# Optimization experiments

Hardware: AMD Instinct MI355X
Metric: run time of the kernel (lower is better)

Reference implementation:

```python
import jax, jax.numpy as jnp
import numpy as np

B, T = 128, 512
V, E, H, A, L = 50000, 256, 512, 64, 2


def setup_inputs() -> dict:
    key = jax.random.key(0)
    ks = jax.random.split(key, 16)
    token_ids = jax.random.randint(ks[0], (B, T), 0, V, dtype=jnp.int32)
    # lengths must be >= 2 so that the source's (len-1)-1 index is valid
    lengths = jnp.clip(jax.random.randint(ks[1], (B,), 0, T, dtype=jnp.int32), 4, T)
    s = 0.05
    inp = {
        "token_ids": token_ids,
        "lengths": lengths,
        "embedding": jax.random.normal(ks[2], (V, E), jnp.float32) * s,
        "Wt": jax.random.normal(ks[3], (A, E), jnp.float32) * s,   # tokens_linear
        "bt": jax.random.normal(ks[4], (A,), jnp.float32) * s,
        "Wq": jax.random.normal(ks[5], (A, H), jnp.float32) * s,   # query_linear
        "bq": jax.random.normal(ks[6], (A,), jnp.float32) * s,
        "v": jax.random.normal(ks[7], (A,), jnp.float32) * s,      # attention_linear weight
        "bv": jax.random.normal(ks[8], (), jnp.float32) * s,       # attention_linear bias
        "gru_Wih0": jax.random.normal(ks[9], (3 * H, A), jnp.float32) * s,
        "gru_Whh0": jax.random.normal(ks[10], (3 * H, H), jnp.float32) * s,
        "gru_bih0": jax.random.normal(ks[11], (3 * H,), jnp.float32) * s,
        "gru_bhh0": jax.random.normal(ks[12], (3 * H,), jnp.float32) * s,
        "gru_Wih1": jax.random.normal(ks[13], (3 * H, H), jnp.float32) * s,
        "gru_Whh1": jax.random.normal(ks[14], (3 * H, H), jnp.float32) * s,
        "gru_bih1": jax.random.normal(ks[15], (3 * H,), jnp.float32) * s,
        "gru_bhh1": jax.random.normal(jax.random.fold_in(key, 99), (3 * H,), jnp.float32) * s,
    }
    return inp


def _gru_cell(x, h, Wih, Whh, bih, bhh):
    gi = x @ Wih.T + bih      # [B, 3H]
    gh = h @ Whh.T + bhh      # [B, 3H]
    i_r, i_z, i_n = jnp.split(gi, 3, axis=-1)
    h_r, h_z, h_n = jnp.split(gh, 3, axis=-1)
    r = jax.nn.sigmoid(i_r + h_r)
    z = jax.nn.sigmoid(i_z + h_z)
    n = jnp.tanh(i_n + r * h_n)
    return (1.0 - z) * n + z * h


def reference(token_ids, lengths, embedding, Wt, bt, Wq, bq, v, bv,
              gru_Wih0, gru_Whh0, gru_bih0, gru_bhh0,
              gru_Wih1, gru_Whh1, gru_bih1, gru_bhh1):
    x = embedding[token_ids]                 # [B, T, E]
    tp = jnp.einsum('bte,ae->bta', x, Wt) + bt   # tokens_linear, [B, T, A]
    pos = jnp.arange(T)

    def step(h, i):
        # query = hidden_state[-1] (zeros at step 0, matching hidden_state=None)
        q = h[-1] @ Wq.T + bq                # [B, A]
        s = jnp.tanh(tp + q[:, None, :]) @ v + bv   # [B, T]
        s = jnp.where(pos[None, :] <= i, s, -jnp.inf)  # growing prefix
        attn = jax.nn.softmax(s, axis=1)
        ctx = jnp.einsum('bt,bta->ba', attn, tp)     # [B, A]
        h0 = _gru_cell(ctx, h[0], gru_Wih0, gru_Whh0, gru_bih0, gru_bhh0)
        h1 = _gru_cell(h0, h[1], gru_Wih1, gru_Whh1, gru_bih1, gru_bhh1)
        return jnp.stack([h0, h1]), h1

    h_init = jnp.zeros((L, B, H), tp.dtype)
    _, outs = jax.lax.scan(step, h_init, jnp.arange(T))   # outs: [T, B, H]
    # source: sequence_lengths = len-1, then index sequence_lengths-1 = len-2
    idx = jnp.clip(lengths - 2, 0, T - 1)
    result = outs[idx, jnp.arange(B)]                     # [B, H]
    return result
```

## Files before the change

kernel.cpp:

```cpp
#include <hip/hip_runtime.h>

#define NB 128
#define NT 512
#define NE 256
#define NH 512
#define NA 64
#define NG 8
#define GB 16

typedef short bf16x8 __attribute__((ext_vector_type(8)));
typedef float f32x4 __attribute__((ext_vector_type(4)));
typedef unsigned short u16x8 __attribute__((ext_vector_type(8)));
typedef unsigned long long u64;

__device__ __forceinline__ unsigned short f2bf(float f){
  unsigned u = __builtin_bit_cast(unsigned, f);
  u = u + 0x7fffu + ((u >> 16) & 1u);
  return (unsigned short)(u >> 16);
}
__device__ __forceinline__ float bf2f(unsigned short h){
  unsigned u = ((unsigned)h) << 16;
  return __builtin_bit_cast(float, u);
}
__device__ __forceinline__ bf16x8 packbf2(f32x4 a, f32x4 b){
  bf16x8 r;
  r[0]=(short)f2bf(a[0]); r[1]=(short)f2bf(a[1]); r[2]=(short)f2bf(a[2]); r[3]=(short)f2bf(a[3]);
  r[4]=(short)f2bf(b[0]); r[5]=(short)f2bf(b[1]); r[6]=(short)f2bf(b[2]); r[7]=(short)f2bf(b[3]);
  return r;
}
__device__ __forceinline__ bf16x8 loadB_f32(const float* p){
  f32x4 a = *(const f32x4*)p;
  f32x4 b = *(const f32x4*)(p + 4);
  return packbf2(a, b);
}
#define MFMA(a,b,c) __builtin_amdgcn_mfma_f32_16x16x32_bf16(a,b,c,0,0,0)

__device__ __forceinline__ float fsig(float x){
  return __builtin_amdgcn_rcpf(1.f + __expf(-x));
}
__device__ __forceinline__ float ftanh(float x){
  float e2 = __expf(2.f * x);
  return 1.f - 2.f * __builtin_amdgcn_rcpf(e2 + 1.f);
}

__device__ __forceinline__ u64 aload(const u64* p){
  return __hip_atomic_load(p, __ATOMIC_RELAXED, __HIP_MEMORY_SCOPE_AGENT);
}
__device__ __forceinline__ void fire(u64* p, u64 v){
  (void)__hip_atomic_exchange(p, v, __ATOMIC_RELAXED, __HIP_MEMORY_SCOPE_AGENT);
}
__device__ __forceinline__ u64 packh(unsigned sq, float a, float b){
  return ((u64)sq << 32) | ((u64)f2bf(b) << 16) | (u64)f2bf(a);
}
__device__ __forceinline__ u64 packf(unsigned sq, float a){
  return ((u64)sq << 32) | (u64)__builtin_bit_cast(unsigned, a);
}

__global__ __launch_bounds__(256) void k_tp(
    const int* __restrict__ tok, const float* __restrict__ emb,
    const float* __restrict__ Wt, const float* __restrict__ bt,
    unsigned short* __restrict__ tp)
{
  const int lane = threadIdx.x & 63;
  const int w = threadIdx.x >> 6;
  const int m16 = lane & 15, quad = lane >> 4;

  bf16x8 wfq[8][4];
#pragma unroll
  for (int kc = 0; kc < 8; kc++)
#pragma unroll
    for (int nt = 0; nt < 4; nt++)
      wfq[kc][nt] = loadB_f32(Wt + (nt*16 + m16)*NE + kc*32 + quad*8);

  float btv[4];
#pragma unroll
  for (int nt = 0; nt < 4; nt++) btv[nt] = bt[nt*16 + m16];

  const int gw = blockIdx.x * 4 + w;
#pragma unroll 1
  for (int it = 0; it < 4; it++){
    const int pt = gw * 4 + it;
    const int pos = pt*16 + m16;
    const long row = (long)tok[pos];
    const float* xrow = emb + row * NE;
    f32x4 acc[4] = {{0,0,0,0},{0,0,0,0},{0,0,0,0},{0,0,0,0}};
#pragma unroll
    for (int kc = 0; kc < 8; kc++){
      bf16x8 af = loadB_f32(xrow + kc*32 + quad*8);
#pragma unroll
      for (int nt = 0; nt < 4; nt++)
        acc[nt] = MFMA(af, wfq[kc][nt], acc[nt]);
    }
#pragma unroll
    for (int nt = 0; nt < 4; nt++)
#pragma unroll
      for (int r = 0; r < 4; r++){
        int posr = pt*16 + quad*4 + r;
        tp[(long)posr * NA + nt*16 + m16] = f2bf(acc[nt][r] + btv[nt]);
      }
  }
}

__global__ __launch_bounds__(256) void k_pack(
    const float* __restrict__ Wq, unsigned short* __restrict__ blob)
{
  const int lane = threadIdx.x & 63, wv = threadIdx.x >> 6;
  const int m16 = lane & 15, quad = lane >> 4;
#pragma unroll
  for (int kc = 0; kc < 16; kc++){
    bf16x8 t = loadB_f32(Wq + (long)(wv*16 + m16)*NH + kc*32 + quad*8);
    *(bf16x8*)&blob[((wv*16 + kc)*64 + lane)*8] = t;
  }
}

struct KArgs {
  const int* len;
  const float* bq; const float* v; const float* bv;
  const float* Wih0; const float* Whh0; const float* bih0; const float* bhh0;
  const float* Wih1; const float* Whh1; const float* bih1; const float* bhh1;
  const unsigned short* tp;
  const unsigned short* wqblob;
  u64* hbuf;
  u64* cbuf;
  float* out;
};

__device__ __forceinline__ void stage_poll(const u64* __restrict__ buf, unsigned sq,
                                           unsigned short (*hs)[64][8], int tid){
  const int lane = tid & 63, wv = tid >> 6;
  const int b = lane & 15, q8 = lane >> 4;
#pragma unroll
  for (int c = 0; c < 4; c++){
    const int kc = wv*4 + c;
    const u64* u0 = buf + (kc*16 + q8*4)*16 + b;
    u64 x0, x1, x2, x3;
    for (;;){
      x0 = aload(u0);      x1 = aload(u0 + 16);
      x2 = aload(u0 + 32); x3 = aload(u0 + 48);
      if ((unsigned)(x0>>32)==sq && (unsigned)(x1>>32)==sq &&
          (unsigned)(x2>>32)==sq && (unsigned)(x3>>32)==sq) break;
      __builtin_amdgcn_s_sleep(1);
    }
    u16x8 d;
    d[0]=(unsigned short)x0; d[1]=(unsigned short)(x0>>16);
    d[2]=(unsigned short)x1; d[3]=(unsigned short)(x1>>16);
    d[4]=(unsigned short)x2; d[5]=(unsigned short)(x2>>16);
    d[6]=(unsigned short)x3; d[7]=(unsigned short)(x3>>16);
    *(u16x8*)&hs[kc][lane][0] = d;
  }
}

__global__ __launch_bounds__(256, 1) void k_main(KArgs A_)
{
  const int tid = threadIdx.x, lane = tid & 63, w = tid >> 6;
  const int g = blockIdx.x & 7, m = blockIdx.x >> 3;
  const int m16 = lane & 15, quad = lane >> 4;

  __shared__ __attribute__((aligned(16))) unsigned short h0s[16][64][8];
  __shared__ __attribute__((aligned(16))) unsigned short h1s[16][64][8];
  __shared__ __attribute__((aligned(16))) float dslab[6][256];
  __shared__ __attribute__((aligned(16))) float qs[16][68];
  __shared__ __attribute__((aligned(16))) float cslab[4][64];
  __shared__ float cden[4];
  __shared__ __attribute__((aligned(16))) unsigned short ctxf[64][16];

  u64* hb = A_.hbuf + (long)g * (4*4096);
  u64* cb = A_.cbuf + (long)g * (2*2*16*72);
  const int b0 = g * GB;

  bf16x8 wf[48], wih0f[2];
  float bhh0v[4], bih0v[4], bhh1v[4], bih1v[4];
  if (w < 3){
    const int r0 = w * NH + m * 16;
#pragma unroll
    for (int kc = 0; kc < 16; kc++){
      wf[kc]    = loadB_f32(A_.Whh0 + (long)(r0 + m16)*NH + kc*32 + quad*8);
      wf[16+kc] = loadB_f32(A_.Whh1 + (long)(r0 + m16)*NH + kc*32 + quad*8);
      wf[32+kc] = loadB_f32(A_.Wih1 + (long)(r0 + m16)*NH + kc*32 + quad*8);
    }
#pragma unroll
    for (int kc = 0; kc < 2; kc++)
      wih0f[kc] = loadB_f32(A_.Wih0 + (r0 + m16)*NA + kc*32 + quad*8);
#pragma unroll
    for (int r = 0; r < 4; r++){
      int d = r0 + quad*4 + r;
      bhh0v[r] = A_.bhh0[d]; bih0v[r] = A_.bih0[d];
      bhh1v[r] = A_.bhh1[d]; bih1v[r] = A_.bih1[d];
    }
  }
  float bqw[4];
#pragma unroll
  for (int r = 0; r < 4; r++) bqw[r] = A_.bq[w*16 + quad*4 + r];

  float vv[16];
#pragma unroll
  for (int jj = 0; jj < 16; jj++) vv[jj] = A_.v[quad*16 + jj];
  const float bvv = A_.bv[0];
  const int ab = m >> 1;
  const int wr = (m & 1)*4 + w;

  int myidx = 0, imax = 0;
#pragma unroll 1
  for (int b = 0; b < GB; b++){
    int L = A_.len[b0 + b];
    int ix = L - 2; ix = ix < 0 ? 0 : (ix > NT-1 ? NT-1 : ix);
    if (b == m16) myidx = ix;
    imax = imax > ix ? imax : ix;
  }

  f32x4 h0p = {0,0,0,0}, h1p = {0,0,0,0};

  {
    u16x8 z = {0,0,0,0,0,0,0,0};
#pragma unroll
    for (int c = 0; c < 4; c++){
      int kc = (tid>>6)*4 + c;
      *(u16x8*)&h0s[kc][lane][0] = z;
      *(u16x8*)&h1s[kc][lane][0] = z;
    }
  }
  __syncthreads();

#pragma unroll 1
  for (int i = 0; i <= imax; i++){
    const int par = i & 1;
    const unsigned sq = (unsigned)(i + 1);

    if (i > 0){
      stage_poll(hb + (long)(2 + ((i-1)&1))*4096, (unsigned)i, h1s, tid);
      __syncthreads();
    }
    {
      f32x4 qa = {0,0,0,0};
#pragma unroll
      for (int kc = 0; kc < 16; kc++){
        bf16x8 b1f = *(const bf16x8*)&h1s[kc][lane][0];
        bf16x8 af = *(const bf16x8*)&A_.wqblob[((w*16 + kc)*64 + lane)*8];
        qa = MFMA(af, b1f, qa);
      }
#pragma unroll
      for (int r = 0; r < 4; r++)
        qs[m16][w*16 + quad*4 + r] = qa[r] + bqw[r];
    }
    __syncthreads();

    {
      float qv[16];
#pragma unroll
      for (int jq = 0; jq < 4; jq++){
        f32x4 t = *(const f32x4*)&qs[ab][quad*16 + jq*4];
        qv[jq*4+0]=t[0]; qv[jq*4+1]=t[1]; qv[jq*4+2]=t[2]; qv[jq*4+3]=t[3];
      }
      float ctxp[16];
#pragma unroll
      for (int jj = 0; jj < 16; jj++) ctxp[jj] = 0.f;
      float denp = 0.f;
      const unsigned short* tpb = A_.tp + (long)(b0 + ab) * NT * NA;
#pragma unroll 1
      for (int c = wr; c*16 <= i; c += 8){
        const int t = c*16 + m16;
        const unsigned short* tpp = tpb + (long)t*NA + quad*16;
        u16x8 ta = *(const u16x8*)tpp;
        u16x8 tb = *(const u16x8*)(tpp + 8);
        float tpf[16];
#pragma unroll
        for (int jj = 0; jj < 8; jj++){ tpf[jj] = bf2f(ta[jj]); tpf[8+jj] = bf2f(tb[jj]); }
        float sp = 0.f;
#pragma unroll
        for (int jj = 0; jj < 16; jj++){
          float x = tpf[jj] + qv[jj];
          sp = fmaf(ftanh(x), vv[jj], sp);
        }
        sp += __shfl_xor(sp, 16);
        sp += __shfl_xor(sp, 32);
        float e = __expf(sp + bvv);
        e = (t <= i) ? e : 0.f;
        denp += e;
#pragma unroll
        for (int jj = 0; jj < 16; jj++) ctxp[jj] = fmaf(e, tpf[jj], ctxp[jj]);
      }
#pragma unroll
      for (int off = 1; off < 64; off <<= 1) denp += __shfl_xor(denp, off);
      denp *= 0.25f;
#pragma unroll
      for (int st = 0; st < 4; st++){
        const int bit = 1 << st;
        const bool up = (lane >> st) & 1;
        const int n2 = (16 >> st) >> 1;
#pragma unroll
        for (int j2 = 0; j2 < 8; j2++){
          if (j2 < n2){
            float keep = up ? ctxp[2*j2+1] : ctxp[2*j2];
            float send = up ? ctxp[2*j2]   : ctxp[2*j2+1];
            float got = __shfl_xor(send, bit);
            ctxp[j2] = keep + got;
          }
        }
      }
      cslab[w][lane] = ctxp[0];
      if (lane == 0) cden[w] = denp;
    }
    __syncthreads();
    if (w == 0){
      float s = cslab[0][lane] + cslab[1][lane] + cslab[2][lane] + cslab[3][lane];
      u64* slot = cb + ((long)(par*2 + (m & 1))*16 + ab)*72;
      fire(slot + lane, packf(sq, s));
      if (lane == 0)
        fire(slot + 64, packf(sq, cden[0]+cden[1]+cden[2]+cden[3]));
    }

    f32x4 gh1 = {0,0,0,0}, g0 = {0,0,0,0};
    if (w < 3){
#pragma unroll
      for (int kc = 0; kc < 16; kc++){
        bf16x8 b1f = *(const bf16x8*)&h1s[kc][lane][0];
        gh1 = MFMA(wf[16+kc], b1f, gh1);
        bf16x8 h0f = *(const bf16x8*)&h0s[kc][lane][0];
        g0  = MFMA(wf[kc], h0f, g0);
      }
#pragma unroll
      for (int r = 0; r < 4; r++){ gh1[r] += bhh1v[r]; g0[r] += bhh0v[r]; }
    } else {
      const u64* c0 = cb + ((long)(par*2 + 0)*16 + m16)*72;
      const u64* c1 = cb + ((long)(par*2 + 1)*16 + m16)*72;
      u64 d0, d1;
      for (;;){
        d0 = aload(c0 + 64); d1 = aload(c1 + 64);
        if ((unsigned)(d0>>32)==sq && (unsigned)(d1>>32)==sq) break;
        __builtin_amdgcn_s_sleep(1);
      }
      const float rdn = __builtin_amdgcn_rcpf(
          __builtin_bit_cast(float,(unsigned)d0) + __builtin_bit_cast(float,(unsigned)d1));
#pragma unroll
      for (int kc = 0; kc < 2; kc++){
        const int a0 = kc*32 + quad*8;
        u64 t0[8], t1[8];
        for (;;){
          bool ok = true;
#pragma unroll
          for (int j = 0; j < 8; j++){ t0[j] = aload(c0 + a0 + j); ok &= ((unsigned)(t0[j]>>32)==sq); }
#pragma unroll
          for (int j = 0; j < 8; j++){ t1[j] = aload(c1 + a0 + j); ok &= ((unsigned)(t1[j]>>32)==sq); }
          if (ok) break;
          __builtin_amdgcn_s_sleep(1);
        }
        u16x8 f;
#pragma unroll
        for (int j = 0; j < 8; j++){
          float s = (__builtin_bit_cast(float,(unsigned)t0[j]) +
                     __builtin_bit_cast(float,(unsigned)t1[j])) * rdn;
          f[j] = f2bf(s);
        }
        *(u16x8*)&ctxf[lane][kc*8] = f;
      }
    }
    __syncthreads();
    if (w < 3){
      f32x4 gi0 = {0,0,0,0};
      bf16x8 cf0 = *(const bf16x8*)&ctxf[lane][0];
      bf16x8 cf1 = *(const bf16x8*)&ctxf[lane][8];
      gi0 = MFMA(wih0f[0], cf0, gi0);
      gi0 = MFMA(wih0f[1], cf1, gi0);
#pragma unroll
      for (int r = 0; r < 4; r++) gi0[r] += bih0v[r];
      *(f32x4*)&dslab[w][lane*4] = g0;
      *(f32x4*)&dslab[3+w][lane*4] = gi0;
    }
    __syncthreads();
    if (w == 3){
      f32x4 ghr = *(f32x4*)&dslab[0][lane*4];
      f32x4 ghz = *(f32x4*)&dslab[1][lane*4];
      f32x4 ghn = *(f32x4*)&dslab[2][lane*4];
      f32x4 gir = *(f32x4*)&dslab[3][lane*4];
      f32x4 giz = *(f32x4*)&dslab[4][lane*4];
      f32x4 gin = *(f32x4*)&dslab[5][lane*4];
      f32x4 hn;
#pragma unroll
      for (int r = 0; r < 4; r++){
        float rr = fsig(gir[r] + ghr[r]);
        float zz = fsig(giz[r] + ghz[r]);
        float nn = ftanh(gin[r] + rr*ghn[r]);
        hn[r] = (1.f - zz)*nn + zz*h0p[r];
      }
      h0p = hn;
      u64* p0 = hb + (long)par*4096 + (m*8 + quad*2)*16 + m16;
      fire(p0,      packh(sq, hn[0], hn[1]));
      fire(p0 + 16, packh(sq, hn[2], hn[3]));
    }

    stage_poll(hb + (long)par*4096, sq, h0s, tid);
    __syncthreads();
    if (w < 3){
      f32x4 gi1 = {0,0,0,0};
#pragma unroll
      for (int kc = 0; kc < 16; kc++){
        bf16x8 hf = *(const bf16x8*)&h0s[kc][lane][0];
        gi1 = MFMA(wf[32+kc], hf, gi1);
      }
#pragma unroll
      for (int r = 0; r < 4; r++) gi1[r] += bih1v[r];
      *(f32x4*)&dslab[w][lane*4] = gh1;
      *(f32x4*)&dslab[3+w][lane*4] = gi1;
    }
    __syncthreads();
    if (w == 3){
      f32x4 ghr = *(f32x4*)&dslab[0][lane*4];
      f32x4 ghz = *(f32x4*)&dslab[1][lane*4];
      f32x4 ghn = *(f32x4*)&dslab[2][lane*4];
      f32x4 gir = *(f32x4*)&dslab[3][lane*4];
      f32x4 giz = *(f32x4*)&dslab[4][lane*4];
      f32x4 gin = *(f32x4*)&dslab[5][lane*4];
      f32x4 hn;
#pragma unroll
      for (int r = 0; r < 4; r++){
        float rr = fsig(gir[r] + ghr[r]);
        float zz = fsig(giz[r] + ghz[r]);
        float nn = ftanh(gin[r] + rr*ghn[r]);
        hn[r] = (1.f - zz)*nn + zz*h1p[r];
      }
      h1p = hn;
      u64* p1 = hb + (long)(2 + par)*4096 + (m*8 + quad*2)*16 + m16;
      fire(p1,      packh(sq, hn[0], hn[1]));
      fire(p1 + 16, packh(sq, hn[2], hn[3]));
      if (i == myidx)
        *(f32x4*)&A_.out[(long)(b0 + m16)*NH + m*16 + quad*4] = hn;
    }
  }
}

extern "C" void kernel_launch(void* const* d_in, const int* in_sizes, int n_in,
                              void* d_out, int out_size, void* d_ws, size_t ws_size,
                              hipStream_t stream)
{
  (void)in_sizes; (void)n_in; (void)out_size; (void)ws_size;
  char* ws = (char*)d_ws;
  unsigned short* tp     = (unsigned short*)ws;
  unsigned short* wqblob = (unsigned short*)(ws + 8388608);
  u64* hbuf = (u64*)(ws + 8388608 + 65536);
  u64* cbuf = hbuf + 8 * (4*4096);

  (void)hipMemsetAsync(hbuf, 0xFF, (size_t)(8*4*4096 + 8*2*2*16*72) * sizeof(u64), stream);

  k_tp<<<dim3(256), dim3(256), 0, stream>>>(
      (const int*)d_in[0], (const float*)d_in[2], (const float*)d_in[3],
      (const float*)d_in[4], tp);
  k_pack<<<dim3(1), dim3(256), 0, stream>>>((const float*)d_in[5], wqblob);

  KArgs ka;
  ka.len  = (const int*)d_in[1];
  ka.bq   = (const float*)d_in[6];
  ka.v    = (const float*)d_in[7];  ka.bv   = (const float*)d_in[8];
  ka.Wih0 = (const float*)d_in[9];  ka.Whh0 = (const float*)d_in[10];
  ka.bih0 = (const float*)d_in[11]; ka.bhh0 = (const float*)d_in[12];
  ka.Wih1 = (const float*)d_in[13]; ka.Whh1 = (const float*)d_in[14];
  ka.bih1 = (const float*)d_in[15]; ka.bhh1 = (const float*)d_in[16];
  ka.tp = tp; ka.wqblob = wqblob;
  ka.hbuf = hbuf; ka.cbuf = cbuf;
  ka.out = (float*)d_out;

  k_main<<<dim3(256), dim3(256), 0, stream>>>(ka);
}
```

Baseline: 7.063 ms.

## Add per-block sentinel flags and contiguous hidden-state layout for cross-block polling

Adds sentinel arrays that each block sets after publishing its hidden-state and context slices. Consumers now spin on these small flags (one wavefront for hidden state, w==3 for context) before doing a single load of the tagged data, instead of every thread polling the full data. The hidden buffer layout also changes so each lane reads four consecutive u64s rather than strided ones. This is meant to cut polling traffic and improve coalescing, at the cost of an extra barrier and an extra flag round trip per stage.

Result: slower. 9.190 ms (+30.1%).

```diff
diff --git a/kernel.cpp b/kernel.cpp
--- a/kernel.cpp
+++ b/kernel.cpp
@@ -122,21 +122,23 @@
   const unsigned short* wqblob;
   u64* hbuf;
   u64* cbuf;
+  u64* hsent;
+  u64* csent;
   float* out;
 };
 
-__device__ __forceinline__ void stage_poll(const u64* __restrict__ buf, unsigned sq,
+__device__ __forceinline__ void stage_load(const u64* __restrict__ buf, unsigned sq,
                                            unsigned short (*hs)[64][8], int tid){
   const int lane = tid & 63, wv = tid >> 6;
   const int b = lane & 15, q8 = lane >> 4;
 #pragma unroll
   for (int c = 0; c < 4; c++){
     const int kc = wv*4 + c;
-    const u64* u0 = buf + (kc*16 + q8*4)*16 + b;
+    const u64* u0 = buf + (kc*4 + q8)*64 + b*4;
     u64 x0, x1, x2, x3;
     for (;;){
-      x0 = aload(u0);      x1 = aload(u0 + 16);
-      x2 = aload(u0 + 32); x3 = aload(u0 + 48);
+      x0 = aload(u0);     x1 = aload(u0 + 1);
+      x2 = aload(u0 + 2); x3 = aload(u0 + 3);
       if ((unsigned)(x0>>32)==sq && (unsigned)(x1>>32)==sq &&
           (unsigned)(x2>>32)==sq && (unsigned)(x3>>32)==sq) break;
       __builtin_amdgcn_s_sleep(1);
@@ -166,6 +168,8 @@
 
   u64* hb = A_.hbuf + (long)g * (4*4096);
   u64* cb = A_.cbuf + (long)g * (2*2*16*72);
+  u64* hsg = A_.hsent + (long)g * 128;
+  u64* csg = A_.csent + (long)g * 64;
   const int b0 = g * GB;
 
   bf16x8 wf[48], wih0f[2];
@@ -227,7 +231,12 @@
     const unsigned sq = (unsigned)(i + 1);
 
     if (i > 0){
-      stage_poll(hb + (long)(2 + ((i-1)&1))*4096, (unsigned)i, h1s, tid);
+      if (w == 0 && lane < 32){
+        const u64* sp = hsg + (long)(2 + ((i-1)&1))*32;
+        while (aload(sp + lane) != (u64)(unsigned)i) __builtin_amdgcn_s_sleep(1);
+      }
+      __syncthreads();
+      stage_load(hb + (long)(2 + ((i-1)&1))*4096, (unsigned)i, h1s, tid);
       __syncthreads();
     }
     {
@@ -307,6 +316,8 @@
       fire(slot + lane, packf(sq, s));
       if (lane == 0)
         fire(slot + 64, packf(sq, cden[0]+cden[1]+cden[2]+cden[3]));
+      if (lane == 0)
+        fire(csg + (par*2 + (m & 1))*16 + ab, (u64)sq);
     }
 
     f32x4 gh1 = {0,0,0,0}, g0 = {0,0,0,0};
@@ -321,6 +332,15 @@
 #pragma unroll
       for (int r = 0; r < 4; r++){ gh1[r] += bhh1v[r]; g0[r] += bhh0v[r]; }
     } else {
+      {
+        const u64* s0 = csg + (par*2 + 0)*16 + m16;
+        const u64* s1 = csg + (par*2 + 1)*16 + m16;
+        for (;;){
+          u64 a = aload(s0), b = aload(s1);
+          if (a == (u64)sq && b == (u64)sq) break;
+          __builtin_amdgcn_s_sleep(1);
+        }
+      }
       const u64* c0 = cb + ((long)(par*2 + 0)*16 + m16)*72;
       const u64* c1 = cb + ((long)(par*2 + 1)*16 + m16)*72;
       u64 d0, d1;
@@ -383,12 +403,19 @@
         hn[r] = (1.f - zz)*nn + zz*h0p[r];
       }
       h0p = hn;
-      u64* p0 = hb + (long)par*4096 + (m*8 + quad*2)*16 + m16;
-      fire(p0,      packh(sq, hn[0], hn[1]));
-      fire(p0 + 16, packh(sq, hn[2], hn[3]));
-    }
-
-    stage_poll(hb + (long)par*4096, sq, h0s, tid);
+      const int dp0 = m*8 + quad*2;
+      u64* p0 = hb + (long)par*4096 + (dp0>>2)*64 + m16*4 + (dp0&3);
+      fire(p0,     packh(sq, hn[0], hn[1]));
+      fire(p0 + 1, packh(sq, hn[2], hn[3]));
+      if (lane == 0) fire(hsg + (long)par*32 + m, (u64)sq);
+    }
+
+    if (w == 0 && lane < 32){
+      const u64* sp = hsg + (long)par*32;
+      while (aload(sp + lane) != (u64)sq) __builtin_amdgcn_s_sleep(1);
+    }
+    __syncthreads();
+    stage_load(hb + (long)par*4096, sq, h0s, tid);
     __syncthreads();
     if (w < 3){
       f32x4 gi1 = {0,0,0,0};
@@ -419,9 +446,11 @@
         hn[r] = (1.f - zz)*nn + zz*h1p[r];
       }
       h1p = hn;
-      u64* p1 = hb + (long)(2 + par)*4096 + (m*8 + quad*2)*16 + m16;
-      fire(p1,      packh(sq, hn[0], hn[1]));
-      fire(p1 + 16, packh(sq, hn[2], hn[3]));
+      const int dp0 = m*8 + quad*2;
+      u64* p1 = hb + (long)(2 + par)*4096 + (dp0>>2)*64 + m16*4 + (dp0&3);
+      fire(p1,     packh(sq, hn[0], hn[1]));
+      fire(p1 + 1, packh(sq, hn[2], hn[3]));
+      if (lane == 0) fire(hsg + (long)(2 + par)*32 + m, (u64)sq);
       if (i == myidx)
         *(f32x4*)&A_.out[(long)(b0 + m16)*NH + m*16 + quad*4] = hn;
     }
@@ -436,10 +465,13 @@
   char* ws = (char*)d_ws;
   unsigned short* tp     = (unsigned short*)ws;
   unsigned short* wqblob = (unsigned short*)(ws + 8388608);
-  u64* hbuf = (u64*)(ws + 8388608 + 65536);
-  u64* cbuf = hbuf + 8 * (4*4096);
-
-  (void)hipMemsetAsync(hbuf, 0xFF, (size_t)(8*4*4096 + 8*2*2*16*72) * sizeof(u64), stream);
+  u64* hbuf  = (u64*)(ws + 8388608 + 65536);
+  u64* cbuf  = hbuf + 8 * (4*4096);
+  u64* hsent = cbuf + 8 * (2*2*16*72);
+  u64* csent = hsent + 8 * 128;
+
+  const size_t tagged = (size_t)(8*4*4096 + 8*2*2*16*72 + 8*128 + 8*64) * sizeof(u64);
+  (void)hipMemsetAsync(hbuf, 0xFF, tagged, stream);
 
   k_tp<<<dim3(256), dim3(256), 0, stream>>>(
       (const int*)d_in[0], (const float*)d_in[2], (const float*)d_in[3],
@@ -455,7 +487,7 @@
   ka.Wih1 = (const float*)d_in[13]; ka.Whh1 = (const float*)d_in[14];
   ka.bih1 = (const float*)d_in[15]; ka.bhh1 = (const float*)d_in[16];
   ka.tp = tp; ka.wqblob = wqblob;
-  ka.hbuf = hbuf; ka.cbuf = cbuf;
+  ka.hbuf = hbuf; ka.cbuf = cbuf; ka.hsent = hsent; ka.csent = csent;
   ka.out = (float*)d_out;
 
   k_main<<<dim3(256), dim3(256), 0, stream>>>(ka);
```

## Add probed fast-path cross-block exchange using workgroup-scope atomics and sc0 loads

Applied to the files above, without the earlier changes.

Adds a startup probe in which the 32 blocks of each batch group check that workgroup-scope exchanges are visible to each other (which holds when they share an L2/XCD). If the probe passes, the per-step hidden-state and context exchanges switch from agent-scope atomics to workgroup-scope stores and sc0 vector loads, with an RMW fallback when polling. The h-buffer layout is also changed so each lane can fetch four tagged words in one contiguous dwordx4 load. The aim is to cut inter-block synchronisation latency in the 512-step recurrence. It adds extra barriers and buffer resets at start and end, and correctness depends on the probe and the cache-coherence assumptions holding.

Measured after the change: 12.47 ms. 76.6% more time.

```diff
diff --git a/kernel.cpp b/kernel.cpp
--- a/kernel.cpp
+++ b/kernel.cpp
@@ -11,7 +11,10 @@
 typedef short bf16x8 __attribute__((ext_vector_type(8)));
 typedef float f32x4 __attribute__((ext_vector_type(4)));
 typedef unsigned short u16x8 __attribute__((ext_vector_type(8)));
+typedef unsigned u32x4 __attribute__((ext_vector_type(4)));
 typedef unsigned long long u64;
+
+#define TAGFF 0xFFFFFFFFFFFFFFFFull
 
 __device__ __forceinline__ unsigned short f2bf(float f){
   unsigned u = __builtin_bit_cast(unsigned, f);
@@ -48,6 +51,28 @@
 }
 __device__ __forceinline__ void fire(u64* p, u64 v){
   (void)__hip_atomic_exchange(p, v, __ATOMIC_RELAXED, __HIP_MEMORY_SCOPE_AGENT);
+}
+__device__ __forceinline__ void fire_f(u64* p, u64 v){
+  (void)__hip_atomic_exchange(p, v, __ATOMIC_RELAXED, __HIP_MEMORY_SCOPE_WORKGROUP);
+}
+__device__ __forceinline__ u64 rmw0(u64* p){
+  return __hip_atomic_fetch_add(p, 0ull, __ATOMIC_RELAXED, __HIP_MEMORY_SCOPE_WORKGROUP);
+}
+__device__ __forceinline__ void load4_sc0(const u64* p, u64& x0, u64& x1, u64& x2, u64& x3){
+  u32x4 a, b;
+  asm volatile("global_load_dwordx4 %0, %2, off sc0\n\t"
+               "global_load_dwordx4 %1, %2, off offset:16 sc0\n\t"
+               "s_waitcnt vmcnt(0)"
+               : "=&v"(a), "=&v"(b) : "v"(p) : "memory");
+  x0 = ((u64)a[1]<<32)|a[0]; x1 = ((u64)a[3]<<32)|a[2];
+  x2 = ((u64)b[1]<<32)|b[0]; x3 = ((u64)b[3]<<32)|b[2];
+}
+__device__ __forceinline__ u64 load1_sc0(const u64* p){
+  u64 x;
+  asm volatile("global_load_dwordx2 %0, %1, off sc0\n\t"
+               "s_waitcnt vmcnt(0)"
+               : "=&v"(x) : "v"(p) : "memory");
+  return x;
 }
 __device__ __forceinline__ u64 packh(unsigned sq, float a, float b){
   return ((u64)sq << 32) | ((u64)f2bf(b) << 16) | (u64)f2bf(a);
@@ -102,8 +127,10 @@
 }
 
 __global__ __launch_bounds__(256) void k_pack(
-    const float* __restrict__ Wq, unsigned short* __restrict__ blob)
+    const float* __restrict__ Wq, unsigned short* __restrict__ blob, u64* nonce)
 {
+  if (threadIdx.x == 0)
+    (void)__hip_atomic_fetch_add(nonce, 1ull, __ATOMIC_RELAXED, __HIP_MEMORY_SCOPE_AGENT);
   const int lane = threadIdx.x & 63, wv = threadIdx.x >> 6;
   const int m16 = lane & 15, quad = lane >> 4;
 #pragma unroll
@@ -122,24 +149,41 @@
   const unsigned short* wqblob;
   u64* hbuf;
   u64* cbuf;
+  u64* ptab;
+  u64* vt1;
+  u64* vt2;
+  u64* nonce;
   float* out;
 };
 
-__device__ __forceinline__ void stage_poll(const u64* __restrict__ buf, unsigned sq,
-                                           unsigned short (*hs)[64][8], int tid){
+__device__ __forceinline__ void stage_load(u64* __restrict__ buf, unsigned sq,
+                                           unsigned short (*hs)[64][8], int tid, bool fast){
   const int lane = tid & 63, wv = tid >> 6;
   const int b = lane & 15, q8 = lane >> 4;
 #pragma unroll
   for (int c = 0; c < 4; c++){
     const int kc = wv*4 + c;
-    const u64* u0 = buf + (kc*16 + q8*4)*16 + b;
+    u64* u0 = buf + (kc*4 + q8)*64 + b*4;
     u64 x0, x1, x2, x3;
-    for (;;){
-      x0 = aload(u0);      x1 = aload(u0 + 16);
-      x2 = aload(u0 + 32); x3 = aload(u0 + 48);
-      if ((unsigned)(x0>>32)==sq && (unsigned)(x1>>32)==sq &&
-          (unsigned)(x2>>32)==sq && (unsigned)(x3>>32)==sq) break;
-      __builtin_amdgcn_s_sleep(1);
+    if (fast){
+      for (;;){
+        load4_sc0(u0, x0, x1, x2, x3);
+        if ((unsigned)(x0>>32)==sq && (unsigned)(x1>>32)==sq &&
+            (unsigned)(x2>>32)==sq && (unsigned)(x3>>32)==sq) break;
+        x0 = rmw0(u0);     x1 = rmw0(u0 + 1);
+        x2 = rmw0(u0 + 2); x3 = rmw0(u0 + 3);
+        if ((unsigned)(x0>>32)==sq && (unsigned)(x1>>32)==sq &&
+            (unsigned)(x2>>32)==sq && (unsigned)(x3>>32)==sq) break;
+        __builtin_amdgcn_s_sleep(1);
+      }
+    } else {
+      for (;;){
+        x0 = aload(u0);     x1 = aload(u0 + 1);
+        x2 = aload(u0 + 2); x3 = aload(u0 + 3);
+        if ((unsigned)(x0>>32)==sq && (unsigned)(x1>>32)==sq &&
+            (unsigned)(x2>>32)==sq && (unsigned)(x3>>32)==sq) break;
+        __builtin_amdgcn_s_sleep(1);
+      }
     }
     u16x8 d;
     d[0]=(unsigned short)x0; d[1]=(unsigned short)(x0>>16);
@@ -163,9 +207,13 @@
   __shared__ __attribute__((aligned(16))) float cslab[4][64];
   __shared__ float cden[4];
   __shared__ __attribute__((aligned(16))) unsigned short ctxf[64][16];
-
-  u64* hb = A_.hbuf + (long)g * (4*4096);
-  u64* cb = A_.cbuf + (long)g * (2*2*16*72);
+  __shared__ int fastflag;
+
+  u64* hb  = A_.hbuf + (long)g * (4*4096);
+  u64* cb  = A_.cbuf + (long)g * (2*2*16*72);
+  u64* pt  = A_.ptab + g*32;
+  u64* vt1 = A_.vt1  + g*32;
+  u64* vt2 = A_.vt2  + g*32;
   const int b0 = g * GB;
 
   bf16x8 wf[48], wih0f[2];
@@ -219,7 +267,45 @@
       *(u16x8*)&h1s[kc][lane][0] = z;
     }
   }
+
+  if (tid == 0){
+    const u64 nn = aload(A_.nonce);
+    int ok = 1;
+    for (int r = 1; r <= 3 && ok; r++){
+      fire_f(pt + m, (nn << 16) | (unsigned)(r*64 + m));
+      for (int j = 0; j < 32 && ok; j++){
+        const u64 want = (nn << 16) | (unsigned)(r*64 + j);
+        int cnt = 0;
+        while (rmw0(pt + j) != want){
+          if (++cnt > 20000){ ok = 0; break; }
+          __builtin_amdgcn_s_sleep(4);
+        }
+      }
+    }
+    fire(vt1 + m, ok ? 1ull : 2ull);
+    int allok = 1;
+    for (int j = 0; j < 32; j++){
+      u64 v;
+      while ((v = aload(vt1 + j)) == 0) __builtin_amdgcn_s_sleep(2);
+      allok &= (v == 1ull);
+    }
+    fastflag = allok;
+  }
   __syncthreads();
+  const bool fast = (fastflag != 0);
+
+  if (fast){
+    fire_f(hb + m*512 + tid*2 + 0, TAGFF);
+    fire_f(hb + m*512 + tid*2 + 1, TAGFF);
+    if (tid < 144) fire_f(cb + m*144 + tid, TAGFF);
+    __syncthreads();
+    if (tid == 0){
+      fire(vt2 + m, 1ull);
+      for (int j = 0; j < 32; j++)
+        while (aload(vt2 + j) == 0) __builtin_amdgcn_s_sleep(2);
+    }
+    __syncthreads();
+  }
 
 #pragma unroll 1
   for (int i = 0; i <= imax; i++){
@@ -227,7 +313,7 @@
     const unsigned sq = (unsigned)(i + 1);
 
     if (i > 0){
-      stage_poll(hb + (long)(2 + ((i-1)&1))*4096, (unsigned)i, h1s, tid);
+      stage_load(hb + (long)(2 + ((i-1)&1))*4096, (unsigned)i, h1s, tid, fast);
       __syncthreads();
     }
     {
@@ -304,9 +390,15 @@
     if (w == 0){
       float s = cslab[0][lane] + cslab[1][lane] + cslab[2][lane] + cslab[3][lane];
       u64* slot = cb + ((long)(par*2 + (m & 1))*16 + ab)*72;
-      fire(slot + lane, packf(sq, s));
-      if (lane == 0)
-        fire(slot + 64, packf(sq, cden[0]+cden[1]+cden[2]+cden[3]));
+      u64 du = packf(sq, s);
+      u64 dd = packf(sq, cden[0]+cden[1]+cden[2]+cden[3]);
+      if (fast){
+        fire_f(slot + lane, du);
+        if (lane == 0) fire_f(slot + 64, dd);
+      } else {
+        fire(slot + lane, du);
+        if (lane == 0) fire(slot + 64, dd);
+      }
     }
 
     f32x4 gh1 = {0,0,0,0}, g0 = {0,0,0,0};
@@ -321,13 +413,23 @@
 #pragma unroll
       for (int r = 0; r < 4; r++){ gh1[r] += bhh1v[r]; g0[r] += bhh0v[r]; }
     } else {
-      const u64* c0 = cb + ((long)(par*2 + 0)*16 + m16)*72;
-      const u64* c1 = cb + ((long)(par*2 + 1)*16 + m16)*72;
+      u64* c0 = cb + ((long)(par*2 + 0)*16 + m16)*72;
+      u64* c1 = cb + ((long)(par*2 + 1)*16 + m16)*72;
       u64 d0, d1;
-      for (;;){
-        d0 = aload(c0 + 64); d1 = aload(c1 + 64);
-        if ((unsigned)(d0>>32)==sq && (unsigned)(d1>>32)==sq) break;
-        __builtin_amdgcn_s_sleep(1);
+      if (fast){
+        for (;;){
+          d0 = load1_sc0(c0 + 64); d1 = load1_sc0(c1 + 64);
+          if ((unsigned)(d0>>32)==sq && (unsigned)(d1>>32)==sq) break;
+          d0 = rmw0(c0 + 64); d1 = rmw0(c1 + 64);
+          if ((unsigned)(d0>>32)==sq && (unsigned)(d1>>32)==sq) break;
+          __builtin_amdgcn_s_sleep(1);
+        }
+      } else {
+        for (;;){
+          d0 = aload(c0 + 64); d1 = aload(c1 + 64);
+          if ((unsigned)(d0>>32)==sq && (unsigned)(d1>>32)==sq) break;
+          __builtin_amdgcn_s_sleep(1);
+        }
       }
       const float rdn = __builtin_amdgcn_rcpf(
           __builtin_bit_cast(float,(unsigned)d0) + __builtin_bit_cast(float,(unsigned)d1));
@@ -335,14 +437,36 @@
       for (int kc = 0; kc < 2; kc++){
         const int a0 = kc*32 + quad*8;
         u64 t0[8], t1[8];
-        for (;;){
-          bool ok = true;
-#pragma unroll
-          for (int j = 0; j < 8; j++){ t0[j] = aload(c0 + a0 + j); ok &= ((unsigned)(t0[j]>>32)==sq); }
-#pragma unroll
-          for (int j = 0; j < 8; j++){ t1[j] = aload(c1 + a0 + j); ok &= ((unsigned)(t1[j]>>32)==sq); }
-          if (ok) break;
-          __builtin_amdgcn_s_sleep(1);
+        if (fast){
+          for (;;){
+            bool ok = true;
+            load4_sc0(c0 + a0,     t0[0], t0[1], t0[2], t0[3]);
+            load4_sc0(c0 + a0 + 4, t0[4], t0[5], t0[6], t0[7]);
+            load4_sc0(c1 + a0,     t1[0], t1[1], t1[2], t1[3]);
+            load4_sc0(c1 + a0 + 4, t1[4], t1[5], t1[6], t1[7]);
+#pragma unroll
+            for (int j = 0; j < 8; j++)
+              ok &= ((unsigned)(t0[j]>>32)==sq) & ((unsigned)(t1[j]>>32)==sq);
+            if (ok) break;
+            ok = true;
+#pragma unroll
+            for (int j = 0; j < 8; j++){
+              t0[j] = rmw0(c0 + a0 + j); ok &= ((unsigned)(t0[j]>>32)==sq);
+              t1[j] = rmw0(c1 + a0 + j); ok &= ((unsigned)(t1[j]>>32)==sq);
+            }
+            if (ok) break;
+            __builtin_amdgcn_s_sleep(1);
+          }
+        } else {
+          for (;;){
+            bool ok = true;
+#pragma unroll
+            for (int j = 0; j < 8; j++){ t0[j] = aload(c0 + a0 + j); ok &= ((unsigned)(t0[j]>>32)==sq); }
+#pragma unroll
+            for (int j = 0; j < 8; j++){ t1[j] = aload(c1 + a0 + j); ok &= ((unsigned)(t1[j]>>32)==sq); }
+            if (ok) break;
+            __builtin_amdgcn_s_sleep(1);
+          }
         }
         u16x8 f;
 #pragma unroll
@@ -383,12 +507,15 @@
         hn[r] = (1.f - zz)*nn + zz*h0p[r];
       }
       h0p = hn;
-      u64* p0 = hb + (long)par*4096 + (m*8 + quad*2)*16 + m16;
-      fire(p0,      packh(sq, hn[0], hn[1]));
-      fire(p0 + 16, packh(sq, hn[2], hn[3]));
-    }
-
-    stage_poll(hb + (long)par*4096, sq, h0s, tid);
+      const int dp0 = m*8 + quad*2;
+      u64* p0 = hb + (long)par*4096 + (dp0>>2)*64 + m16*4 + (dp0&3);
+      u64 va = packh(sq, hn[0], hn[1]);
+      u64 vb = packh(sq, hn[2], hn[3]);
+      if (fast){ fire_f(p0, va); fire_f(p0 + 1, vb); }
+      else     { fire(p0, va);   fire(p0 + 1, vb); }
+    }
+
+    stage_load(hb + (long)par*4096, sq, h0s, tid, fast);
     __syncthreads();
     if (w < 3){
       f32x4 gi1 = {0,0,0,0};
@@ -419,12 +546,27 @@
         hn[r] = (1.f - zz)*nn + zz*h1p[r];
       }
       h1p = hn;
-      u64* p1 = hb + (long)(2 + par)*4096 + (m*8 + quad*2)*16 + m16;
-      fire(p1,      packh(sq, hn[0], hn[1]));
-      fire(p1 + 16, packh(sq, hn[2], hn[3]));
+      const int dp0 = m*8 + quad*2;
+      u64* p1 = hb + (long)(2 + par)*4096 + (dp0>>2)*64 + m16*4 + (dp0&3);
+      u64 va = packh(sq, hn[0], hn[1]);
+      u64 vb = packh(sq, hn[2], hn[3]);
+      if (fast){ fire_f(p1, va); fire_f(p1 + 1, vb); }
+      else     { fire(p1, va);   fire(p1 + 1, vb); }
       if (i == myidx)
         *(f32x4*)&A_.out[(long)(b0 + m16)*NH + m*16 + quad*4] = hn;
     }
+  }
+
+  if (fast){
+    if (tid == 0){
+      fire(vt2 + m, 2ull);
+      for (int j = 0; j < 32; j++)
+        while (aload(vt2 + j) < 2ull) __builtin_amdgcn_s_sleep(2);
+    }
+    __syncthreads();
+    fire_f(hb + m*512 + tid*2 + 0, TAGFF);
+    fire_f(hb + m*512 + tid*2 + 1, TAGFF);
+    if (tid < 144) fire_f(cb + m*144 + tid, TAGFF);
   }
 }
 
@@ -436,15 +578,20 @@
   char* ws = (char*)d_ws;
   unsigned short* tp     = (unsigned short*)ws;
   unsigned short* wqblob = (unsigned short*)(ws + 8388608);
-  u64* hbuf = (u64*)(ws + 8388608 + 65536);
-  u64* cbuf = hbuf + 8 * (4*4096);
+  u64* hbuf  = (u64*)(ws + 8388608 + 65536);
+  u64* cbuf  = hbuf + 8 * (4*4096);
+  u64* ptab  = cbuf + 8 * (2*2*16*72);
+  u64* vt1   = ptab + 256;
+  u64* vt2   = vt1 + 256;
+  u64* nonce = vt2 + 256;
 
   (void)hipMemsetAsync(hbuf, 0xFF, (size_t)(8*4*4096 + 8*2*2*16*72) * sizeof(u64), stream);
+  (void)hipMemsetAsync(ptab, 0, (size_t)(3*256) * sizeof(u64), stream);
 
   k_tp<<<dim3(256), dim3(256), 0, stream>>>(
       (const int*)d_in[0], (const float*)d_in[2], (const float*)d_in[3],
       (const float*)d_in[4], tp);
-  k_pack<<<dim3(1), dim3(256), 0, stream>>>((const float*)d_in[5], wqblob);
+  k_pack<<<dim3(1), dim3(256), 0, stream>>>((const float*)d_in[5], wqblob, nonce);
 
   KArgs ka;
   ka.len  = (const int*)d_in[1];
@@ -456,6 +603,7 @@
   ka.bih1 = (const float*)d_in[15]; ka.bhh1 = (const float*)d_in[16];
   ka.tp = tp; ka.wqblob = wqblob;
   ka.hbuf = hbuf; ka.cbuf = cbuf;
+  ka.ptab = ptab; ka.vt1 = vt1; ka.vt2 = vt2; ka.nonce = nonce;
   ka.out = (float*)d_out;
 
   k_main<<<dim3(256), dim3(256), 0, stream>>>(ka);
```

## Reorder GRU matmuls to overlap polling, relayout hidden-state mailbox, add backoff

Applied to the files above, without the earlier changes.

The Whh0·h0 matmul moves to the start of each step, before waiting on the previous layer-1 hidden state, and the Whh1·h1 matmul moves to just before polling for the new layer-0 state. Both now run while the block waits on other blocks instead of on the critical path. The hidden-state mailbox layout changes so each lane polls four contiguous u64 words rather than words spaced 16 apart, which should cut cache lines touched per poll. Spin loops gain exponential sleep backoff, which may lower contention but can add wake-up latency.

New measurement: 6.863 ms. 1.03x faster.

```diff
diff --git a/kernel.cpp b/kernel.cpp
--- a/kernel.cpp
+++ b/kernel.cpp
@@ -41,6 +41,13 @@
 __device__ __forceinline__ float ftanh(float x){
   float e2 = __expf(2.f * x);
   return 1.f - 2.f * __builtin_amdgcn_rcpf(e2 + 1.f);
+}
+
+__device__ __forceinline__ void sleep_bk(int bk){
+  if (bk <= 0)      __builtin_amdgcn_s_sleep(1);
+  else if (bk == 1) __builtin_amdgcn_s_sleep(2);
+  else if (bk == 2) __builtin_amdgcn_s_sleep(4);
+  else              __builtin_amdgcn_s_sleep(8);
 }
 
 __device__ __forceinline__ u64 aload(const u64* p){
@@ -125,21 +132,23 @@
   float* out;
 };
 
-__device__ __forceinline__ void stage_poll(const u64* __restrict__ buf, unsigned sq,
+__device__ __forceinline__ void stage_load(const u64* __restrict__ buf, unsigned sq,
                                            unsigned short (*hs)[64][8], int tid){
   const int lane = tid & 63, wv = tid >> 6;
   const int b = lane & 15, q8 = lane >> 4;
 #pragma unroll
   for (int c = 0; c < 4; c++){
     const int kc = wv*4 + c;
-    const u64* u0 = buf + (kc*16 + q8*4)*16 + b;
+    const u64* u0 = buf + (kc*4 + q8)*64 + b*4;
     u64 x0, x1, x2, x3;
+    int bk = 0;
     for (;;){
-      x0 = aload(u0);      x1 = aload(u0 + 16);
-      x2 = aload(u0 + 32); x3 = aload(u0 + 48);
+      x0 = aload(u0);     x1 = aload(u0 + 1);
+      x2 = aload(u0 + 2); x3 = aload(u0 + 3);
       if ((unsigned)(x0>>32)==sq && (unsigned)(x1>>32)==sq &&
           (unsigned)(x2>>32)==sq && (unsigned)(x3>>32)==sq) break;
-      __builtin_amdgcn_s_sleep(1);
+      sleep_bk(bk);
+      if (bk < 3) bk++;
     }
     u16x8 d;
     d[0]=(unsigned short)x0; d[1]=(unsigned short)(x0>>16);
@@ -226,8 +235,18 @@
     const int par = i & 1;
     const unsigned sq = (unsigned)(i + 1);
 
+    f32x4 g0 = {0,0,0,0};
+    if (w < 3){
+#pragma unroll
+      for (int kc = 0; kc < 16; kc++){
+        bf16x8 h0f = *(const bf16x8*)&h0s[kc][lane][0];
+        g0 = MFMA(wf[kc], h0f, g0);
+      }
+#pragma unroll
+      for (int r = 0; r < 4; r++) g0[r] += bhh0v[r];
+    }
     if (i > 0){
-      stage_poll(hb + (long)(2 + ((i-1)&1))*4096, (unsigned)i, h1s, tid);
+      stage_load(hb + (long)(2 + ((i-1)&1))*4096, (unsigned)i, h1s, tid);
       __syncthreads();
     }
     {
@@ -309,25 +328,18 @@
         fire(slot + 64, packf(sq, cden[0]+cden[1]+cden[2]+cden[3]));
     }
 
-    f32x4 gh1 = {0,0,0,0}, g0 = {0,0,0,0};
-    if (w < 3){
-#pragma unroll
-      for (int kc = 0; kc < 16; kc++){
-        bf16x8 b1f = *(const bf16x8*)&h1s[kc][lane][0];
-        gh1 = MFMA(wf[16+kc], b1f, gh1);
-        bf16x8 h0f = *(const bf16x8*)&h0s[kc][lane][0];
-        g0  = MFMA(wf[kc], h0f, g0);
-      }
-#pragma unroll
-      for (int r = 0; r < 4; r++){ gh1[r] += bhh1v[r]; g0[r] += bhh0v[r]; }
-    } else {
+    if (w == 3){
       const u64* c0 = cb + ((long)(par*2 + 0)*16 + m16)*72;
       const u64* c1 = cb + ((long)(par*2 + 1)*16 + m16)*72;
       u64 d0, d1;
-      for (;;){
-        d0 = aload(c0 + 64); d1 = aload(c1 + 64);
-        if ((unsigned)(d0>>32)==sq && (unsigned)(d1>>32)==sq) break;
-        __builtin_amdgcn_s_sleep(1);
+      {
+        int bk = 0;
+        for (;;){
+          d0 = aload(c0 + 64); d1 = aload(c1 + 64);
+          if ((unsigned)(d0>>32)==sq && (unsigned)(d1>>32)==sq) break;
+          sleep_bk(bk);
+          if (bk < 3) bk++;
+        }
       }
       const float rdn = __builtin_amdgcn_rcpf(
           __builtin_bit_cast(float,(unsigned)d0) + __builtin_bit_cast(float,(unsigned)d1));
@@ -335,6 +347,7 @@
       for (int kc = 0; kc < 2; kc++){
         const int a0 = kc*32 + quad*8;
         u64 t0[8], t1[8];
+        int bk = 0;
         for (;;){
           bool ok = true;
 #pragma unroll
@@ -342,7 +355,8 @@
 #pragma unroll
           for (int j = 0; j < 8; j++){ t1[j] = aload(c1 + a0 + j); ok &= ((unsigned)(t1[j]>>32)==sq); }
           if (ok) break;
-          __builtin_amdgcn_s_sleep(1);
+          sleep_bk(bk);
+          if (bk < 3) bk++;
         }
         u16x8 f;
 #pragma unroll
@@ -383,12 +397,23 @@
         hn[r] = (1.f - zz)*nn + zz*h0p[r];
       }
       h0p = hn;
-      u64* p0 = hb + (long)par*4096 + (m*8 + quad*2)*16 + m16;
-      fire(p0,      packh(sq, hn[0], hn[1]));
-      fire(p0 + 16, packh(sq, hn[2], hn[3]));
-    }
-
-    stage_poll(hb + (long)par*4096, sq, h0s, tid);
+      const int dp0 = m*8 + quad*2;
+      u64* p0 = hb + (long)par*4096 + (dp0>>2)*64 + m16*4 + (dp0&3);
+      fire(p0,     packh(sq, hn[0], hn[1]));
+      fire(p0 + 1, packh(sq, hn[2], hn[3]));
+    }
+
+    f32x4 gh1 = {0,0,0,0};
+    if (w < 3){
+#pragma unroll
+      for (int kc = 0; kc < 16; kc++){
+        bf16x8 b1f = *(const bf16x8*)&h1s[kc][lane][0];
+        gh1 = MFMA(wf[16+kc], b1f, gh1);
+      }
+#pragma unroll
+      for (int r = 0; r < 4; r++) gh1[r] += bhh1v[r];
+    }
+    stage_load(hb + (long)par*4096, sq, h0s, tid);
     __syncthreads();
     if (w < 3){
       f32x4 gi1 = {0,0,0,0};
@@ -419,9 +444,10 @@
         hn[r] = (1.f - zz)*nn + zz*h1p[r];
       }
       h1p = hn;
-      u64* p1 = hb + (long)(2 + par)*4096 + (m*8 + quad*2)*16 + m16;
-      fire(p1,      packh(sq, hn[0], hn[1]));
-      fire(p1 + 16, packh(sq, hn[2], hn[3]));
+      const int dp0 = m*8 + quad*2;
+      u64* p1 = hb + (long)(2 + par)*4096 + (dp0>>2)*64 + m16*4 + (dp0&3);
+      fire(p1,     packh(sq, hn[0], hn[1]));
+      fire(p1 + 1, packh(sq, hn[2], hn[3]));
       if (i == myidx)
         *(f32x4*)&A_.out[(long)(b0 + m16)*NH + m*16 + quad*4] = hn;
     }
```
